# Performance work log

Hardware: AMD Instinct MI355X
Metric: run time of the kernel (lower is better)

Reference implementation:

```python
import jax, jax.numpy as jnp
import numpy as np

VOCAB = 100000
DIM = 128
B = 32768
K = 16


def setup_inputs() -> dict:
    key = jax.random.key(0)
    k1, k2, k3, k4, k5 = jax.random.split(key, 5)
    init_range = 0.5 / DIM
    word_emb = jax.random.uniform(k1, (VOCAB, DIM), jnp.float32, -init_range, init_range)
    con_emb = jax.random.uniform(k2, (VOCAB, DIM), jnp.float32, -init_range, init_range)
    centrals_words = jax.random.randint(k3, (B,), 0, VOCAB, jnp.int64 if jax.config.jax_enable_x64 else jnp.int32)
    pos_context = jax.random.randint(k4, (B,), 0, VOCAB, centrals_words.dtype)
    neg_context = jax.random.randint(k5, (B, K), 0, VOCAB, centrals_words.dtype)
    return {
        "centrals_words": centrals_words,
        "pos_context": pos_context,
        "neg_context": neg_context,
        "word_emb": word_emb,
        "con_emb": con_emb,
    }


def reference(centrals_words, pos_context, neg_context, word_emb, con_emb):
    # Gathers
    w = word_emb[centrals_words]        # [B, D]
    c = con_emb[pos_context]            # [B, D]
    n = con_emb[neg_context]            # [B, K, D]
    # Positive score: dot over D
    pos_score = jnp.sum(w * c, axis=1)              # [B]
    pos_loss = jax.nn.log_sigmoid(pos_score)        # [B]
    # Negative scores: bmm [B,K,D] @ [B,D,1] -> [B,K]
    neg_score = jnp.einsum('bkd,bd->bk', n, w)      # [B, K]
    neg_loss = jnp.sum(jax.nn.log_sigmoid(-neg_score), axis=1)  # [B]
    loss = -jnp.mean(pos_loss + neg_loss)
    return loss
```

## Files before the change

### kernel.cpp

```cpp
#include <hip/hip_runtime.h>
#include <hip/hip_fp16.h>


constexpr int Bn = 32768;
constexpr int Kn = 16;
constexpr int WPB = 4;
constexpr int NBLK = Bn / WPB;
constexpr int VOCAB = 100000;
constexpr int DIM = 128;
constexpr size_t CONV_OFF = 65536;

__device__ __forceinline__ float log_sigmoid_fast(float x) {
  return fminf(x, 0.0f) - __logf(1.0f + __expf(-fabsf(x)));
}

template<int M, int C>
__device__ __forceinline__ void tree_step(float* v, int lane) {
  const bool hi = (lane & M) != 0;
  const int H = C / 2;
#pragma unroll
  for (int j = 0; j < H; ++j) {
    float send = hi ? v[j] : v[j + H];
    float keep = hi ? v[j + H] : v[j];
    v[j] = keep + __shfl_xor(send, M, 64);
  }
}

__global__ __launch_bounds__(256) void convert_con(
    const float4* __restrict__ in, ushort4* __restrict__ out, int n4)
{
  int i = blockIdx.x * 256 + threadIdx.x;
  if (i >= n4) return;
  float4 v = in[i];
  ushort4 o;
  o.x = __half_as_ushort(__float2half(v.x));
  o.y = __half_as_ushort(__float2half(v.y));
  o.z = __half_as_ushort(__float2half(v.z));
  o.w = __half_as_ushort(__float2half(v.w));
  out[i] = o;
}

__global__ __launch_bounds__(256) void skipgram_main(
    const int* __restrict__ centrals,
    const int* __restrict__ pos_ctx,
    const int* __restrict__ neg_ctx,
    const float* __restrict__ word_emb,
    const __half2* __restrict__ con_half,
    float* __restrict__ block_sums)
{
  const int lane = threadIdx.x & 63;
  int b = blockIdx.x * WPB + (threadIdx.x >> 6);
  b = __builtin_amdgcn_readfirstlane(b);

  const float2* __restrict__ W = reinterpret_cast<const float2*>(word_emb);

  const int cw = centrals[b];
  const int pc = pos_ctx[b];
  int ni[Kn];
#pragma unroll
  for (int k = 0; k < Kn; ++k) ni[k] = neg_ctx[b * Kn + k];

  const float2 wv = W[(size_t)cw * 64 + lane];
  const __half2 cvh = con_half[(size_t)pc * 64 + lane];
  __half2 nvh[Kn];
#pragma unroll
  for (int k = 0; k < Kn; ++k) nvh[k] = con_half[(size_t)ni[k] * 64 + lane];

  float v[Kn];
#pragma unroll
  for (int k = 0; k < Kn; ++k) {
    const float2 nf = __half22float2(nvh[k]);
    v[k] = fmaf(wv.x, nf.x, wv.y * nf.y);
  }

  tree_step<1, 16>(v, lane);
  tree_step<2,  8>(v, lane);
  tree_step<4,  4>(v, lane);
  tree_step<8,  2>(v, lane);
  float s = v[0];
  s += __shfl_xor(s, 16, 64);
  s += __shfl_xor(s, 32, 64);

  float nls = log_sigmoid_fast(-s);
  nls += __shfl_xor(nls, 1, 64);
  nls += __shfl_xor(nls, 2, 64);
  nls += __shfl_xor(nls, 4, 64);
  nls += __shfl_xor(nls, 8, 64);

  const float2 cf = __half22float2(cvh);
  float pp = fmaf(wv.x, cf.x, wv.y * cf.y);
  pp += __shfl_xor(pp,  1, 64);
  pp += __shfl_xor(pp,  2, 64);
  pp += __shfl_xor(pp,  4, 64);
  pp += __shfl_xor(pp,  8, 64);
  pp += __shfl_xor(pp, 16, 64);
  pp += __shfl_xor(pp, 32, 64);

  const float acc = log_sigmoid_fast(pp) + nls;

  __shared__ float smem[WPB];
  if (lane == 0) smem[threadIdx.x >> 6] = acc;
  __syncthreads();
  if (threadIdx.x == 0)
    block_sums[blockIdx.x] = (smem[0] + smem[1]) + (smem[2] + smem[3]);
}

__global__ __launch_bounds__(256) void skipgram_reduce(
    const float* __restrict__ block_sums, float* __restrict__ out)
{
  float s = 0.0f;
#pragma unroll
  for (int i = 0; i < NBLK / 256; ++i) s += block_sums[i * 256 + threadIdx.x];
  s += __shfl_xor(s,  1, 64);
  s += __shfl_xor(s,  2, 64);
  s += __shfl_xor(s,  4, 64);
  s += __shfl_xor(s,  8, 64);
  s += __shfl_xor(s, 16, 64);
  s += __shfl_xor(s, 32, 64);
  __shared__ float smem[4];
  const int lane = threadIdx.x & 63;
  if (lane == 0) smem[threadIdx.x >> 6] = s;
  __syncthreads();
  if (threadIdx.x == 0) {
    float t = (smem[0] + smem[1]) + (smem[2] + smem[3]);
    out[0] = -t * (1.0f / (float)Bn);
  }
}

extern "C" void kernel_launch(void* const* d_in, const int* in_sizes, int n_in,
                              void* d_out, int out_size, void* d_ws, size_t ws_size,
                              hipStream_t stream) {
  const int*   centrals = (const int*)d_in[0];
  const int*   pos_ctx  = (const int*)d_in[1];
  const int*   neg_ctx  = (const int*)d_in[2];
  const float* word_emb = (const float*)d_in[3];
  const float* con_emb  = (const float*)d_in[4];
  float*       out      = (float*)d_out;

  float*   block_sums = (float*)d_ws;
  __half2* con_half   = (__half2*)((char*)d_ws + CONV_OFF);

  const int n4 = VOCAB * DIM / 4;
  convert_con<<<(n4 + 255) / 256, 256, 0, stream>>>(
      (const float4*)con_emb, (ushort4*)con_half, n4);

  skipgram_main<<<NBLK, 256, 0, stream>>>(centrals, pos_ctx, neg_ctx,
                                          word_emb, con_half, block_sums);

  skipgram_reduce<<<1, 256, 0, stream>>>(block_sums, out);
}
```

Before: 144.4 us.

## Quantize context embeddings to scaled FP8 e4m3 and fold final reduction into atomics

The per-call conversion pass now stores the context embedding table as scaled software-encoded e4m3 bytes instead of fp16, which halves both the conversion write traffic and the gathered bytes in the main kernel. The main kernel decodes the bytes with bit manipulation. The separate reduce kernel is dropped: each block atomically adds its scaled partial sum into the output, which the conversion kernel zeroes. This cuts memory traffic and one launch, at the cost of much coarser precision (underflow to zero below a threshold) and a nondeterministic summation order from the atomics.

New measurement: 224.4 us. +55.4%, slower.

```diff
diff --git a/kernel.cpp b/kernel.cpp
--- a/kernel.cpp
+++ b/kernel.cpp
@@ -8,7 +8,6 @@
 constexpr int NBLK = Bn / WPB;
 constexpr int VOCAB = 100000;
 constexpr int DIM = 128;
-constexpr size_t CONV_OFF = 65536;
 
 __device__ __forceinline__ float log_sigmoid_fast(float x) {
   return fminf(x, 0.0f) - __logf(1.0f + __expf(-fabsf(x)));
@@ -26,18 +25,33 @@
   }
 }
 
+__device__ __forceinline__ unsigned int enc_e4m3(float c) {
+  unsigned short h = __half_as_ushort(__float2half(c * 256.0f));
+  unsigned short hr = (unsigned short)(h + 0x40);
+  int ex = (hr >> 10) & 0x1f;
+  if (ex < 9) return 0u;
+  return (unsigned int)(((hr >> 8) & 0x80) |
+                        (((hr - 0x2000) >> 7) & 0x7f));
+}
+
+__device__ __forceinline__ float2 dec2_e4m3(unsigned short t) {
+  unsigned int x  = ((unsigned int)t & 0xffu) | (((unsigned int)t & 0xff00u) << 8);
+  unsigned int h2 = ((x & 0x00800080u) << 8) | ((x & 0x007f007fu) << 7);
+  __half2 hv = *reinterpret_cast<__half2*>(&h2);
+  return __half22float2(hv);
+}
+
 __global__ __launch_bounds__(256) void convert_con(
-    const float4* __restrict__ in, ushort4* __restrict__ out, int n4)
+    const float4* __restrict__ in, unsigned int* __restrict__ out, int n4,
+    float* __restrict__ loss_out)
 {
   int i = blockIdx.x * 256 + threadIdx.x;
+  if (i == 0) loss_out[0] = 0.0f;
   if (i >= n4) return;
   float4 v = in[i];
-  ushort4 o;
-  o.x = __half_as_ushort(__float2half(v.x));
-  o.y = __half_as_ushort(__float2half(v.y));
-  o.z = __half_as_ushort(__float2half(v.z));
-  o.w = __half_as_ushort(__float2half(v.w));
-  out[i] = o;
+  unsigned int b = enc_e4m3(v.x) | (enc_e4m3(v.y) << 8) |
+                   (enc_e4m3(v.z) << 16) | (enc_e4m3(v.w) << 24);
+  out[i] = b;
 }
 
 __global__ __launch_bounds__(256) void skipgram_main(
@@ -45,8 +59,8 @@
     const int* __restrict__ pos_ctx,
     const int* __restrict__ neg_ctx,
     const float* __restrict__ word_emb,
-    const __half2* __restrict__ con_half,
-    float* __restrict__ block_sums)
+    const unsigned short* __restrict__ con8,
+    float* __restrict__ loss_out)
 {
   const int lane = threadIdx.x & 63;
   int b = blockIdx.x * WPB + (threadIdx.x >> 6);
@@ -61,15 +75,15 @@
   for (int k = 0; k < Kn; ++k) ni[k] = neg_ctx[b * Kn + k];
 
   const float2 wv = W[(size_t)cw * 64 + lane];
-  const __half2 cvh = con_half[(size_t)pc * 64 + lane];
-  __half2 nvh[Kn];
+  const unsigned short cvb = con8[(size_t)pc * 64 + lane];
+  unsigned short nvb[Kn];
 #pragma unroll
-  for (int k = 0; k < Kn; ++k) nvh[k] = con_half[(size_t)ni[k] * 64 + lane];
+  for (int k = 0; k < Kn; ++k) nvb[k] = con8[(size_t)ni[k] * 64 + lane];
 
   float v[Kn];
 #pragma unroll
   for (int k = 0; k < Kn; ++k) {
-    const float2 nf = __half22float2(nvh[k]);
+    const float2 nf = dec2_e4m3(nvb[k]);
     v[k] = fmaf(wv.x, nf.x, wv.y * nf.y);
   }
 
@@ -87,7 +101,7 @@
   nls += __shfl_xor(nls, 4, 64);
   nls += __shfl_xor(nls, 8, 64);
 
-  const float2 cf = __half22float2(cvh);
+  const float2 cf = dec2_e4m3(cvb);
   float pp = fmaf(wv.x, cf.x, wv.y * cf.y);
   pp += __shfl_xor(pp,  1, 64);
   pp += __shfl_xor(pp,  2, 64);
@@ -101,29 +115,9 @@
   __shared__ float smem[WPB];
   if (lane == 0) smem[threadIdx.x >> 6] = acc;
   __syncthreads();
-  if (threadIdx.x == 0)
-    block_sums[blockIdx.x] = (smem[0] + smem[1]) + (smem[2] + smem[3]);
-}
-
-__global__ __launch_bounds__(256) void skipgram_reduce(
-    const float* __restrict__ block_sums, float* __restrict__ out)
-{
-  float s = 0.0f;
-#pragma unroll
-  for (int i = 0; i < NBLK / 256; ++i) s += block_sums[i * 256 + threadIdx.x];
-  s += __shfl_xor(s,  1, 64);
-  s += __shfl_xor(s,  2, 64);
-  s += __shfl_xor(s,  4, 64);
-  s += __shfl_xor(s,  8, 64);
-  s += __shfl_xor(s, 16, 64);
-  s += __shfl_xor(s, 32, 64);
-  __shared__ float smem[4];
-  const int lane = threadIdx.x & 63;
-  if (lane == 0) smem[threadIdx.x >> 6] = s;
-  __syncthreads();
   if (threadIdx.x == 0) {
-    float t = (smem[0] + smem[1]) + (smem[2] + smem[3]);
-    out[0] = -t * (1.0f / (float)Bn);
+    const float t = (smem[0] + smem[1]) + (smem[2] + smem[3]);
+    atomicAdd(loss_out, t * (-1.0f / (float)Bn));
   }
 }
 
@@ -137,15 +131,13 @@
   const float* con_emb  = (const float*)d_in[4];
   float*       out      = (float*)d_out;
 
-  float*   block_sums = (float*)d_ws;
-  __half2* con_half   = (__half2*)((char*)d_ws + CONV_OFF);
+  unsigned int* con_fp8 = (unsigned int*)d_ws;
 
   const int n4 = VOCAB * DIM / 4;
   convert_con<<<(n4 + 255) / 256, 256, 0, stream>>>(
-      (const float4*)con_emb, (ushort4*)con_half, n4);
+      (const float4*)con_emb, con_fp8, n4, out);
 
   skipgram_main<<<NBLK, 256, 0, stream>>>(centrals, pos_ctx, neg_ctx,
-                                          word_emb, con_half, block_sums);
-
-  skipgram_reduce<<<1, 256, 0, stream>>>(block_sums, out);
+                                          word_emb,
+                                          (const unsigned short*)con_fp8, out);
 }
```
